# Performance work log

Hardware: AMD Instinct MI355X
Metric: run time of the kernel (lower is better)

The kernel has to match this reference:

```python
import jax, jax.numpy as jnp
import numpy as np
from jax import lax

B, S, DM = 4, 4096, 1024
H, P, R = 16, 32, 8
D = DM // H  # head_dim = 64
K_SEL = 4


def setup_inputs() -> dict:
    key = jax.random.key(0)
    ks = jax.random.split(key, 6)
    x = jax.random.normal(ks[0], (B, S, DM), dtype=jnp.float32)
    K_state = jax.random.normal(ks[1], (H, P, R, D), dtype=jnp.float32) / np.sqrt(D)
    V_state = jax.random.normal(ks[2], (H, P, R, D), dtype=jnp.float32) / np.sqrt(D)
    W_router = jax.random.normal(ks[3], (H, D, P), dtype=jnp.float32) / np.sqrt(D)
    W_out = jax.random.normal(ks[4], (DM, DM), dtype=jnp.float32) / np.sqrt(DM)
    b_out = jnp.zeros((DM,), dtype=jnp.float32)
    return {"x": x, "K_state": K_state, "V_state": V_state,
            "W_router": W_router, "W_out": W_out, "b_out": b_out, "k": K_SEL}


def reference(x, K_state, V_state, W_router, W_out, b_out, k):
    b, s, dm = x.shape
    h, p, r, d = K_state.shape
    xh = x.reshape(b, s, h, d)  # per-head token features

    # Router: top-k partition selection per token per head.
    logits = jnp.einsum('bshd,hdp->bshp', xh, W_router)
    topv = lax.top_k(logits, k)[0]            # [b,s,h,k]
    thresh = topv[..., -1:]                   # k-th largest logit
    neg_inf = jnp.array(-jnp.inf, dtype=logits.dtype)
    gates = jax.nn.softmax(jnp.where(logits >= thresh, logits, neg_inf), axis=-1)  # [b,s,h,p], zero off top-k

    # Attention over state rows within each partition (masked-dense == sparse gather math).
    scale = jnp.asarray(1.0 / np.sqrt(d), dtype=x.dtype)
    scores = jnp.einsum('bshd,hprd->bshpr', xh, K_state) * scale
    attn = jax.nn.softmax(scores, axis=-1)    # softmax over rows r within a partition

    # Gate-weighted combine of per-partition attention outputs, fused to avoid [b,s,h,p,d].
    w = attn * gates[..., None]               # [b,s,h,p,r]
    heads = jnp.einsum('bshpr,hprd->bshd', w, V_state)

    out = heads.reshape(b, s, dm) @ W_out + b_out
    return out
```

## Files before the change

kernel.cpp:

```cpp
#include <hip/hip_runtime.h>
#include <hip/hip_bf16.h>

#define BB 4
#define SS 4096
#define DM 1024
#define HH 16
#define PP 32
#define RR 8
#define DD 64
#define NTOK (BB*SS)
#define MM NTOK
#define NN DM
#define KK DM

typedef __attribute__((ext_vector_type(8))) short short8;
typedef __attribute__((ext_vector_type(4))) float floatx4;

static __device__ inline short f2bf(float f) {
    union { __hip_bfloat16 b; short s; } u; u.b = __float2bfloat16(f); return u.s;
}
static __device__ inline short8 pack8(float4 lo, float4 hi) {
    short8 r;
    r[0] = f2bf(lo.x); r[1] = f2bf(lo.y); r[2] = f2bf(lo.z); r[3] = f2bf(lo.w);
    r[4] = f2bf(hi.x); r[5] = f2bf(hi.y); r[6] = f2bf(hi.z); r[7] = f2bf(hi.w);
    return r;
}

static __device__ inline unsigned bfr(float f) {
    unsigned u = __float_as_uint(f);
    return u + 0x7fffu + ((u >> 16) & 1u);
}
static __device__ inline int pk2(float a, float b) {
    return __builtin_amdgcn_perm(bfr(b), bfr(a), 0x07060302);
}
static __device__ inline short8 pk8(float4 lo, float4 hi) {
    union { short8 s; int i[4]; } r;
    r.i[0] = pk2(lo.x, lo.y); r.i[1] = pk2(lo.z, lo.w);
    r.i[2] = pk2(hi.x, hi.y); r.i[3] = pk2(hi.z, hi.w);
    return r.s;
}

__global__ __launch_bounds__(256) void pre_fused(const float* __restrict__ x,
                                                 const float* __restrict__ Wr,
                                                 const int* __restrict__ kp,
                                                 const float* __restrict__ Wo,
                                                 const float* __restrict__ Kst,
                                                 const float* __restrict__ Vst,
                                                 float* __restrict__ gates_g,
                                                 __hip_bfloat16* __restrict__ wsw,
                                                 __hip_bfloat16* __restrict__ kfrag,
                                                 __hip_bfloat16* __restrict__ vfrag,
                                                 __hip_bfloat16* __restrict__ xbf) {
    const int bx = blockIdx.x;

    if (bx >= 4096) {
        if (bx < 4608) {
            int tid = (bx - 4096) * 256 + threadIdx.x;
            int l = tid & 63;
            int kblk = (tid >> 6) & 31;
            int ntile = tid >> 11;
            int col = ntile * 16 + (l & 15);
            int krow = kblk * 32 + (l >> 4) * 8;
#pragma unroll
            for (int j = 0; j < 8; ++j)
                wsw[(size_t)tid * 8 + j] = __float2bfloat16(Wo[(size_t)(krow + j) * NN + col]);
        } else if (bx < 4864) {
            int tid = (bx - 4608) * 256 + threadIdx.x;
            int arr = tid >> 15;
            int idx = tid & 32767;
            int h = idx >> 11, blk = (idx >> 6) & 31, fl = idx & 63;
            int fm = fl & 15, fk = fl >> 4;
            short8 val;
            short* dst;
            if (arr == 0) {
                int mt = blk >> 1, kb = blk & 1;
                int pr = mt * 16 + fm, d0 = kb * 32 + fk * 8;
                const float* src = Kst + ((size_t)h * 256 + pr) * 64 + d0;
                float4 lo = *(const float4*)src, hi = *(const float4*)(src + 4);
                val = pack8(lo, hi);
                dst = (short*)kfrag + (size_t)idx * 8;
            } else {
                int mt = blk >> 3, kb = blk & 7;
                int d = mt * 16 + fm, pr0 = kb * 32 + fk * 8;
                const float* src = Vst + ((size_t)h * 256 + pr0) * 64 + d;
#pragma unroll
                for (int j = 0; j < 8; ++j) val[j] = f2bf(src[j * 64]);
                dst = (short*)vfrag + (size_t)idx * 8;
            }
            *(short8*)dst = val;
        } else {
            int xid = bx - 4864;
            int tile = xid & 255, h = xid >> 8;
            int lane = threadIdx.x & 63, w = threadIdx.x >> 6;
            int l15 = lane & 15, l4 = lane >> 4;
            const float* srcb = x + (size_t)(tile * 64 + w * 16 + l15) * DM + h * 64 + l4 * 8;
            short* dstb = (short*)xbf + ((size_t)((h * 256 + tile) * 8 + w * 2) * 512) + lane * 8;
#pragma unroll
            for (int kb = 0; kb < 2; ++kb) {
                float4 lo = *(const float4*)(srcb + kb * 32);
                float4 hi = *(const float4*)(srcb + kb * 32 + 4);
                *(short8*)(dstb + kb * 512) = pk8(lo, hi);
            }
        }
        return;
    }

    __shared__ __align__(16) char smem[26624];
    float (*xs)[68] = (float (*)[68])smem;
    float (*Lg)[36] = (float (*)[36])(smem + 17408);

    const int lane = threadIdx.x & 63;
    const int w = threadIdx.x >> 6;
    const int l15 = lane & 15, l4 = lane >> 4;
    const int tile = bx & 255;
    const int h = bx >> 8;
    const int t0 = tile * 64;

    {
        int row = threadIdx.x >> 2, q = threadIdx.x & 3;
        const float4* src = (const float4*)(x + (size_t)(t0 + row) * DM + h * 64 + q * 16);
        float4 v0 = src[0], v1 = src[1], v2 = src[2], v3 = src[3];
        float4* dst = (float4*)&xs[row][q * 16];
        dst[0] = v0; dst[1] = v1; dst[2] = v2; dst[3] = v3;
    }

    const int p = lane & 31, dh = lane >> 5;
    float wreg[32];
    {
        const float* wrp = Wr + (size_t)h * (DD * PP) + dh * 32 * PP + p;
#pragma unroll
        for (int dd = 0; dd < 32; ++dd) wreg[dd] = wrp[dd * PP];
    }
    const int kkv = kp[0];

    __syncthreads();

    for (int it = 0; it < 16; it += 2) {
        const int ta = w * 16 + it;
        const int tb = ta + 1;
        float la = 0.f, lb = 0.f;
#pragma unroll
        for (int j = 0; j < 8; ++j) {
            float4 qa = *(const float4*)&xs[ta][dh * 32 + 4 * j];
            float4 qb = *(const float4*)&xs[tb][dh * 32 + 4 * j];
            la += qa.x * wreg[4 * j];     lb += qb.x * wreg[4 * j];
            la += qa.y * wreg[4 * j + 1]; lb += qb.y * wreg[4 * j + 1];
            la += qa.z * wreg[4 * j + 2]; lb += qb.z * wreg[4 * j + 2];
            la += qa.w * wreg[4 * j + 3]; lb += qb.w * wreg[4 * j + 3];
        }
        la += __shfl_xor(la, 32);
        lb += __shfl_xor(lb, 32);
        if (lane < 32) {
            Lg[ta][lane] = la;
            Lg[tb][lane] = lb;
        }
    }
    __syncthreads();

    float thresh = 0.f, a1 = 0.f;
    if (lane < 16) {
        int t = w * 16 + lane;
        float lgr[32];
        const float4* lrow = (const float4*)&Lg[t][0];
#pragma unroll
        for (int c = 0; c < 8; ++c) {
            float4 q4 = lrow[c];
            lgr[4 * c] = q4.x; lgr[4 * c + 1] = q4.y; lgr[4 * c + 2] = q4.z; lgr[4 * c + 3] = q4.w;
        }
        float aa = -INFINITY, b2 = -INFINITY, c3 = -INFINITY, d4 = -INFINITY;
#pragma unroll
        for (int pp = 0; pp < 32; ++pp) {
            float v = lgr[pp];
            float na = fmaxf(aa, v); v = fminf(aa, v); aa = na;
            float nb = fmaxf(b2, v); v = fminf(b2, v); b2 = nb;
            float nc = fmaxf(c3, v); v = fminf(c3, v); c3 = nc;
            d4 = fmaxf(d4, v);
        }
        thresh = (kkv >= 4) ? d4 : (kkv == 3 ? c3 : (kkv == 2 ? b2 : aa));
        a1 = aa;
    }
    thresh = __shfl(thresh, l15);
    a1     = __shfl(a1, l15);

    {
        const int t = w * 16 + l15;
        const int p8 = l4 * 8;
        const float4* lrow = (const float4*)&Lg[t][p8];
        float4 qa = lrow[0], qb = lrow[1];
        float e0 = (qa.x >= thresh) ? __expf(qa.x - a1) : 0.f;
        float e1 = (qa.y >= thresh) ? __expf(qa.y - a1) : 0.f;
        float e2 = (qa.z >= thresh) ? __expf(qa.z - a1) : 0.f;
        float e3 = (qa.w >= thresh) ? __expf(qa.w - a1) : 0.f;
        float e4 = (qb.x >= thresh) ? __expf(qb.x - a1) : 0.f;
        float e5 = (qb.y >= thresh) ? __expf(qb.y - a1) : 0.f;
        float e6 = (qb.z >= thresh) ? __expf(qb.z - a1) : 0.f;
        float e7 = (qb.w >= thresh) ? __expf(qb.w - a1) : 0.f;
        float part = ((e0 + e1) + (e2 + e3)) + ((e4 + e5) + (e6 + e7));
        part += __shfl_xor(part, 16);
        part += __shfl_xor(part, 32);
        float inv = 1.f / part;
        float* gb = gates_g + ((size_t)(h * 256 + tile) * 32) * 64 + t;
        gb[(p8 + 0) * 64] = e0 * inv;
        gb[(p8 + 1) * 64] = e1 * inv;
        gb[(p8 + 2) * 64] = e2 * inv;
        gb[(p8 + 3) * 64] = e3 * inv;
        gb[(p8 + 4) * 64] = e4 * inv;
        gb[(p8 + 5) * 64] = e5 * inv;
        gb[(p8 + 6) * 64] = e6 * inv;
        gb[(p8 + 7) * 64] = e7 * inv;
    }
}

__global__ __launch_bounds__(256, 3) void attn_mm(const __hip_bfloat16* __restrict__ xbf,
                                                  const __hip_bfloat16* __restrict__ kfrag,
                                                  const __hip_bfloat16* __restrict__ vfrag,
                                                  const float* __restrict__ gates_g,
                                                  __hip_bfloat16* __restrict__ hb) {
    __shared__ __align__(16) short wf[16384];

    const int lane = threadIdx.x & 63;
    const int w = threadIdx.x >> 6;
    const int l15 = lane & 15, l4 = lane >> 4;
    const int t0 = blockIdx.x * 64;
    const int h = blockIdx.y;

    const float* gb = gates_g + ((size_t)(h * 256 + blockIdx.x) * 32) * 64;
    float gv[4][4];
#pragma unroll
    for (int mi = 0; mi < 4; ++mi) {
        const int pidx = (w * 4 + mi) * 2 + (l4 >> 1);
#pragma unroll
        for (int nt = 0; nt < 4; ++nt)
            gv[mi][nt] = gb[pidx * 64 + nt * 16 + l15];
    }

    const short* xbase = (const short*)xbf + ((size_t)(h * 256 + blockIdx.x) * 8) * 512 + lane * 8;
    short8 xb[4][2];
#pragma unroll
    for (int nt = 0; nt < 4; ++nt)
#pragma unroll
        for (int kb = 0; kb < 2; ++kb)
            xb[nt][kb] = *(const short8*)(xbase + (nt * 2 + kb) * 512);
    short8 ka[4][2];
#pragma unroll
    for (int mi = 0; mi < 4; ++mi)
#pragma unroll
        for (int kb = 0; kb < 2; ++kb)
            ka[mi][kb] = *(const short8*)((const short*)kfrag +
                          ((size_t)(h * 32 + (w * 4 + mi) * 2 + kb) * 512 + lane * 8));

    floatx4 acc[4][4] = {};
#pragma unroll
    for (int kb = 0; kb < 2; ++kb)
#pragma unroll
        for (int mi = 0; mi < 4; ++mi)
#pragma unroll
            for (int nt = 0; nt < 4; ++nt)
                acc[mi][nt] = __builtin_amdgcn_mfma_f32_16x16x32_bf16(ka[mi][kb], xb[nt][kb], acc[mi][nt], 0, 0, 0);

#pragma unroll
    for (int mi = 0; mi < 4; ++mi) {
        const int mt = w * 4 + mi;
#pragma unroll
        for (int nt = 0; nt < 4; ++nt) {
            float g = gv[mi][nt];
            float s0 = acc[mi][nt][0] * 0.125f;
            float s1 = acc[mi][nt][1] * 0.125f;
            float s2 = acc[mi][nt][2] * 0.125f;
            float s3 = acc[mi][nt][3] * 0.125f;
            float mx = fmaxf(fmaxf(s0, s1), fmaxf(s2, s3));
            mx = fmaxf(mx, __shfl_xor(mx, 16));
            float e0 = __expf(s0 - mx), e1 = __expf(s1 - mx);
            float e2 = __expf(s2 - mx), e3 = __expf(s3 - mx);
            float loc = (e0 + e1) + (e2 + e3);
            float se = loc + __shfl_xor(loc, 16);
            float ws = g / se;
            int2 pk;
            pk.x = pk2(e0 * ws, e1 * ws);
            pk.y = pk2(e2 * ws, e3 * ws);
            int off = (((mt & 1) * 2 + (l4 >> 1)) * 16 + l15) * 8 + (l4 & 1) * 4;
            *(int2*)&wf[(nt * 8 + (mt >> 1)) * 512 + off] = pk;
        }
    }
    __syncthreads();

    floatx4 h4[4] = {};
#pragma unroll
    for (int kb = 0; kb < 8; ++kb) {
        short8 va = *(const short8*)((const short*)vfrag +
                      ((size_t)(h * 32 + w * 8 + kb) * 512 + lane * 8));
#pragma unroll
        for (int nt = 0; nt < 4; ++nt) {
            short8 wb = *(const short8*)&wf[(nt * 8 + kb) * 512 + lane * 8];
            h4[nt] = __builtin_amdgcn_mfma_f32_16x16x32_bf16(va, wb, h4[nt], 0, 0, 0);
        }
    }
#pragma unroll
    for (int nt = 0; nt < 4; ++nt) {
        int t = t0 + nt * 16 + l15;
        int2 pk;
        pk.x = pk2(h4[nt][0], h4[nt][1]);
        pk.y = pk2(h4[nt][2], h4[nt][3]);
        *(int2*)((short*)hb + (size_t)t * DM + h * 64 + w * 16 + l4 * 4) = pk;
    }
}

__global__ __launch_bounds__(512, 4) void gemm_v8(const __hip_bfloat16* __restrict__ Abf,
                                                  const __hip_bfloat16* __restrict__ Bsw,
                                                  const float* __restrict__ bias,
                                                  float* __restrict__ C) {
    __shared__ __align__(16) short As[2][8192];
    const int lane = threadIdx.x & 63;
    const int wave = threadIdx.x >> 6;
    const int wm = wave >> 2, wn = wave & 3;

    const int wg  = blockIdx.y * 8 + blockIdx.x;
    const int xcd = wg & 7;
    const int loc = wg >> 3;
    const int bm0 = (xcd * 16 + (loc >> 3)) * 128;
    const int bn0 = (loc & 7) * 128;

    const int l15 = lane & 15, l4 = lane >> 4;

    const short* Ap = (const short*)Abf;
    const short* Bp = (const short*)Bsw;

    int crow[2], ck8[2];
#pragma unroll
    for (int j = 0; j < 2; ++j) {
        int c = (wave * 2 + j) * 64 + lane;
        int row = c >> 3;
        crow[j] = row;
        ck8[j] = ((c & 7) ^ (row & 7)) * 8;
    }

    int boff[2];
#pragma unroll
    for (int nt = 0; nt < 2; ++nt)
        boff[nt] = (((bn0 >> 4) + wn * 2 + nt) * 32) * 512 + lane * 8;

    const int axor = l15 & 7;
    int arow[4];
#pragma unroll
    for (int mt = 0; mt < 4; ++mt)
        arow[mt] = (wm * 64 + mt * 16 + l15) * 64;
    const int ak0 = (l4 ^ axor) * 8;
    const int ak1 = ((4 + l4) ^ axor) * 8;

    floatx4 acc[4][2] = {};

#pragma unroll
    for (int j = 0; j < 2; ++j)
        __builtin_amdgcn_global_load_lds(
            (const __attribute__((address_space(1))) unsigned int*)
                (Ap + (size_t)(bm0 + crow[j]) * KK + ck8[j]),
            (__attribute__((address_space(3))) unsigned int*)&As[0][(wave * 2 + j) * 512],
            16, 0, 0);
    short8 bA[2];
#pragma unroll
    for (int nt = 0; nt < 2; ++nt)
        bA[nt] = *(const short8*)(Bp + boff[nt]);
    __syncthreads();

    for (int step = 0; step < 16; ++step) {
        const int cur = step & 1;
        const int nxt = cur ^ 1;

        short8 bB[2];
#pragma unroll
        for (int nt = 0; nt < 2; ++nt)
            bB[nt] = *(const short8*)(Bp + boff[nt] + (size_t)(2 * step + 1) * 512);

        short8 bN[2];
        if (step < 15) {
#pragma unroll
            for (int nt = 0; nt < 2; ++nt)
                bN[nt] = *(const short8*)(Bp + boff[nt] + (size_t)(2 * step + 2) * 512);
#pragma unroll
            for (int j = 0; j < 2; ++j)
                __builtin_amdgcn_global_load_lds(
                    (const __attribute__((address_space(1))) unsigned int*)
                        (Ap + (size_t)(bm0 + crow[j]) * KK + (step + 1) * 64 + ck8[j]),
                    (__attribute__((address_space(3))) unsigned int*)&As[nxt][(wave * 2 + j) * 512],
                    16, 0, 0);
        }

        short8 a0[4];
#pragma unroll
        for (int mt = 0; mt < 4; ++mt)
            a0[mt] = *(const short8*)&As[cur][arow[mt] + ak0];
#pragma unroll
        for (int mt = 0; mt < 4; ++mt)
#pragma unroll
            for (int nt = 0; nt < 2; ++nt)
                acc[mt][nt] = __builtin_amdgcn_mfma_f32_16x16x32_bf16(a0[mt], bA[nt], acc[mt][nt], 0, 0, 0);

        short8 a1[4];
#pragma unroll
        for (int mt = 0; mt < 4; ++mt)
            a1[mt] = *(const short8*)&As[cur][arow[mt] + ak1];
#pragma unroll
        for (int mt = 0; mt < 4; ++mt)
#pragma unroll
            for (int nt = 0; nt < 2; ++nt)
                acc[mt][nt] = __builtin_amdgcn_mfma_f32_16x16x32_bf16(a1[mt], bB[nt], acc[mt][nt], 0, 0, 0);

        if (step < 15) {
#pragma unroll
            for (int nt = 0; nt < 2; ++nt)
                bA[nt] = bN[nt];
        }
        __syncthreads();
    }

#pragma unroll
    for (int nt = 0; nt < 2; ++nt) {
        const int col = bn0 + wn * 32 + nt * 16 + l15;
        const float bv = bias[col];
#pragma unroll
        for (int mt = 0; mt < 4; ++mt) {
            const int row0 = bm0 + wm * 64 + mt * 16 + l4 * 4;
#pragma unroll
            for (int i = 0; i < 4; ++i)
                C[(size_t)(row0 + i) * NN + col] = acc[mt][nt][i] + bv;
        }
    }
}

extern "C" void kernel_launch(void* const* d_in, const int* in_sizes, int n_in,
                              void* d_out, int out_size, void* d_ws, size_t ws_size,
                              hipStream_t stream) {
    const float* x   = (const float*)d_in[0];
    const float* Kst = (const float*)d_in[1];
    const float* Vst = (const float*)d_in[2];
    const float* Wr  = (const float*)d_in[3];
    const float* Wo  = (const float*)d_in[4];
    const float* bo  = (const float*)d_in[5];
    const int*   kp  = (const int*)d_in[6];
    float* out = (float*)d_out;

    __hip_bfloat16* hb    = (__hip_bfloat16*)d_ws;
    __hip_bfloat16* wsw   = hb + (size_t)MM * KK;
    __hip_bfloat16* kfrag = wsw + (size_t)KK * NN;
    __hip_bfloat16* vfrag = kfrag + 16 * 32 * 512;
    float* gates_g = (float*)(vfrag + 16 * 32 * 512);
    __hip_bfloat16* xbf = (__hip_bfloat16*)d_out;

    pre_fused<<<dim3(8960), 256, 0, stream>>>(x, Wr, kp, Wo, Kst, Vst,
                                              gates_g, wsw, kfrag, vfrag, xbf);
    attn_mm<<<dim3(NTOK / 64, HH), 256, 0, stream>>>(xbf, kfrag, vfrag, gates_g, hb);
    gemm_v8<<<dim3(NN / 128, MM / 128), 512, 0, stream>>>(hb, wsw, bo, out);
}
```

Before: 219.3 us.

## Fold x bf16 conversion into router blocks and widen attention kernel to 8 waves

The bf16 conversion of x, which previously ran in separate extra blocks of pre_fused, now runs inside the router blocks that already read the same x tile, so the grid shrinks from 8960 to 4864 blocks. The router logit loop processes four tokens per iteration instead of two, for more ILP. The attention kernel moves from 256 to 512 threads per block: each wave handles two partition m-tiles and half the token n-tiles, which halves per-wave register accumulators and raises parallelism at the cost of more VGPR pressure per block under launch_bounds(512,4).

```diff
diff --git a/kernel.cpp b/kernel.cpp
--- a/kernel.cpp
+++ b/kernel.cpp
@@ -64,7 +64,7 @@
 #pragma unroll
             for (int j = 0; j < 8; ++j)
                 wsw[(size_t)tid * 8 + j] = __float2bfloat16(Wo[(size_t)(krow + j) * NN + col]);
-        } else if (bx < 4864) {
+        } else {
             int tid = (bx - 4608) * 256 + threadIdx.x;
             int arr = tid >> 15;
             int idx = tid & 32767;
@@ -88,19 +88,6 @@
                 dst = (short*)vfrag + (size_t)idx * 8;
             }
             *(short8*)dst = val;
-        } else {
-            int xid = bx - 4864;
-            int tile = xid & 255, h = xid >> 8;
-            int lane = threadIdx.x & 63, w = threadIdx.x >> 6;
-            int l15 = lane & 15, l4 = lane >> 4;
-            const float* srcb = x + (size_t)(tile * 64 + w * 16 + l15) * DM + h * 64 + l4 * 8;
-            short* dstb = (short*)xbf + ((size_t)((h * 256 + tile) * 8 + w * 2) * 512) + lane * 8;
-#pragma unroll
-            for (int kb = 0; kb < 2; ++kb) {
-                float4 lo = *(const float4*)(srcb + kb * 32);
-                float4 hi = *(const float4*)(srcb + kb * 32 + 4);
-                *(short8*)(dstb + kb * 512) = pk8(lo, hi);
-            }
         }
         return;
     }
@@ -124,6 +111,17 @@
         dst[0] = v0; dst[1] = v1; dst[2] = v2; dst[3] = v3;
     }
 
+    {
+        const float* srcb = x + (size_t)(t0 + w * 16 + l15) * DM + h * 64 + l4 * 8;
+        short* dstb = (short*)xbf + ((size_t)((h * 256 + tile) * 8 + w * 2) * 512) + lane * 8;
+#pragma unroll
+        for (int kb = 0; kb < 2; ++kb) {
+            float4 lo = *(const float4*)(srcb + kb * 32);
+            float4 hi = *(const float4*)(srcb + kb * 32 + 4);
+            *(short8*)(dstb + kb * 512) = pk8(lo, hi);
+        }
+    }
+
     const int p = lane & 31, dh = lane >> 5;
     float wreg[32];
     {
@@ -135,24 +133,33 @@
 
     __syncthreads();
 
-    for (int it = 0; it < 16; it += 2) {
+    for (int it = 0; it < 16; it += 4) {
         const int ta = w * 16 + it;
-        const int tb = ta + 1;
-        float la = 0.f, lb = 0.f;
+        float la = 0.f, lb = 0.f, lc = 0.f, ld = 0.f;
 #pragma unroll
         for (int j = 0; j < 8; ++j) {
-            float4 qa = *(const float4*)&xs[ta][dh * 32 + 4 * j];
-            float4 qb = *(const float4*)&xs[tb][dh * 32 + 4 * j];
+            float4 qa = *(const float4*)&xs[ta + 0][dh * 32 + 4 * j];
+            float4 qb = *(const float4*)&xs[ta + 1][dh * 32 + 4 * j];
+            float4 qc = *(const float4*)&xs[ta + 2][dh * 32 + 4 * j];
+            float4 qd = *(const float4*)&xs[ta + 3][dh * 32 + 4 * j];
             la += qa.x * wreg[4 * j];     lb += qb.x * wreg[4 * j];
+            lc += qc.x * wreg[4 * j];     ld += qd.x * wreg[4 * j];
             la += qa.y * wreg[4 * j + 1]; lb += qb.y * wreg[4 * j + 1];
+            lc += qc.y * wreg[4 * j + 1]; ld += qd.y * wreg[4 * j + 1];
             la += qa.z * wreg[4 * j + 2]; lb += qb.z * wreg[4 * j + 2];
+            lc += qc.z * wreg[4 * j + 2]; ld += qd.z * wreg[4 * j + 2];
             la += qa.w * wreg[4 * j + 3]; lb += qb.w * wreg[4 * j + 3];
+            lc += qc.w * wreg[4 * j + 3]; ld += qd.w * wreg[4 * j + 3];
         }
         la += __shfl_xor(la, 32);
         lb += __shfl_xor(lb, 32);
+        lc += __shfl_xor(lc, 32);
+        ld += __shfl_xor(ld, 32);
         if (lane < 32) {
-            Lg[ta][lane] = la;
-            Lg[tb][lane] = lb;
+            Lg[ta + 0][lane] = la;
+            Lg[ta + 1][lane] = lb;
+            Lg[ta + 2][lane] = lc;
+            Lg[ta + 3][lane] = ld;
         }
     }
     __syncthreads();
@@ -211,11 +218,11 @@
     }
 }
 
-__global__ __launch_bounds__(256, 3) void attn_mm(const __hip_bfloat16* __restrict__ xbf,
-                                                  const __hip_bfloat16* __restrict__ kfrag,
-                                                  const __hip_bfloat16* __restrict__ vfrag,
-                                                  const float* __restrict__ gates_g,
-                                                  __hip_bfloat16* __restrict__ hb) {
+__global__ __launch_bounds__(512, 4) void attn_mm8(const __hip_bfloat16* __restrict__ xbf,
+                                                   const __hip_bfloat16* __restrict__ kfrag,
+                                                   const __hip_bfloat16* __restrict__ vfrag,
+                                                   const float* __restrict__ gates_g,
+                                                   __hip_bfloat16* __restrict__ hb) {
     __shared__ __align__(16) short wf[16384];
 
     const int lane = threadIdx.x & 63;
@@ -225,10 +232,10 @@
     const int h = blockIdx.y;
 
     const float* gb = gates_g + ((size_t)(h * 256 + blockIdx.x) * 32) * 64;
-    float gv[4][4];
-#pragma unroll
-    for (int mi = 0; mi < 4; ++mi) {
-        const int pidx = (w * 4 + mi) * 2 + (l4 >> 1);
+    float gv[2][4];
+#pragma unroll
+    for (int mi = 0; mi < 2; ++mi) {
+        const int pidx = (w * 2 + mi) * 2 + (l4 >> 1);
 #pragma unroll
         for (int nt = 0; nt < 4; ++nt)
             gv[mi][nt] = gb[pidx * 64 + nt * 16 + l15];
@@ -241,26 +248,26 @@
 #pragma unroll
         for (int kb = 0; kb < 2; ++kb)
             xb[nt][kb] = *(const short8*)(xbase + (nt * 2 + kb) * 512);
-    short8 ka[4][2];
-#pragma unroll
-    for (int mi = 0; mi < 4; ++mi)
+    short8 ka[2][2];
+#pragma unroll
+    for (int mi = 0; mi < 2; ++mi)
 #pragma unroll
         for (int kb = 0; kb < 2; ++kb)
             ka[mi][kb] = *(const short8*)((const short*)kfrag +
-                          ((size_t)(h * 32 + (w * 4 + mi) * 2 + kb) * 512 + lane * 8));
-
-    floatx4 acc[4][4] = {};
+                          ((size_t)(h * 32 + (w * 2 + mi) * 2 + kb) * 512 + lane * 8));
+
+    floatx4 acc[2][4] = {};
 #pragma unroll
     for (int kb = 0; kb < 2; ++kb)
 #pragma unroll
-        for (int mi = 0; mi < 4; ++mi)
+        for (int mi = 0; mi < 2; ++mi)
 #pragma unroll
             for (int nt = 0; nt < 4; ++nt)
                 acc[mi][nt] = __builtin_amdgcn_mfma_f32_16x16x32_bf16(ka[mi][kb], xb[nt][kb], acc[mi][nt], 0, 0, 0);
 
 #pragma unroll
-    for (int mi = 0; mi < 4; ++mi) {
-        const int mt = w * 4 + mi;
+    for (int mi = 0; mi < 2; ++mi) {
+        const int mt = w * 2 + mi;
 #pragma unroll
         for (int nt = 0; nt < 4; ++nt) {
             float g = gv[mi][nt];
@@ -284,24 +291,26 @@
     }
     __syncthreads();
 
-    floatx4 h4[4] = {};
+    const int dt = w & 3;
+    const int nt0 = (w >> 2) * 2;
+    floatx4 h4[2] = {};
 #pragma unroll
     for (int kb = 0; kb < 8; ++kb) {
         short8 va = *(const short8*)((const short*)vfrag +
-                      ((size_t)(h * 32 + w * 8 + kb) * 512 + lane * 8));
-#pragma unroll
-        for (int nt = 0; nt < 4; ++nt) {
-            short8 wb = *(const short8*)&wf[(nt * 8 + kb) * 512 + lane * 8];
-            h4[nt] = __builtin_amdgcn_mfma_f32_16x16x32_bf16(va, wb, h4[nt], 0, 0, 0);
-        }
-    }
-#pragma unroll
-    for (int nt = 0; nt < 4; ++nt) {
-        int t = t0 + nt * 16 + l15;
+                      ((size_t)(h * 32 + dt * 8 + kb) * 512 + lane * 8));
+#pragma unroll
+        for (int j = 0; j < 2; ++j) {
+            short8 wb = *(const short8*)&wf[((nt0 + j) * 8 + kb) * 512 + lane * 8];
+            h4[j] = __builtin_amdgcn_mfma_f32_16x16x32_bf16(va, wb, h4[j], 0, 0, 0);
+        }
+    }
+#pragma unroll
+    for (int j = 0; j < 2; ++j) {
+        int t = t0 + (nt0 + j) * 16 + l15;
         int2 pk;
-        pk.x = pk2(h4[nt][0], h4[nt][1]);
-        pk.y = pk2(h4[nt][2], h4[nt][3]);
-        *(int2*)((short*)hb + (size_t)t * DM + h * 64 + w * 16 + l4 * 4) = pk;
+        pk.x = pk2(h4[j][0], h4[j][1]);
+        pk.y = pk2(h4[j][2], h4[j][3]);
+        *(int2*)((short*)hb + (size_t)t * DM + h * 64 + dt * 16 + l4 * 4) = pk;
     }
 }
 
@@ -446,8 +455,8 @@
     float* gates_g = (float*)(vfrag + 16 * 32 * 512);
     __hip_bfloat16* xbf = (__hip_bfloat16*)d_out;
 
-    pre_fused<<<dim3(8960), 256, 0, stream>>>(x, Wr, kp, Wo, Kst, Vst,
+    pre_fused<<<dim3(4864), 256, 0, stream>>>(x, Wr, kp, Wo, Kst, Vst,
                                               gates_g, wsw, kfrag, vfrag, xbf);
-    attn_mm<<<dim3(NTOK / 64, HH), 256, 0, stream>>>(xbf, kfrag, vfrag, gates_g, hb);
+    attn_mm8<<<dim3(NTOK / 64, HH), 512, 0, stream>>>(xbf, kfrag, vfrag, gates_g, hb);
     gemm_v8<<<dim3(NN / 128, MM / 128), 512, 0, stream>>>(hb, wsw, bo, out);
 }
```

Measured after the change: 220.3 us. Within noise of the previous version (+0.4%).
